# Performance work log

Hardware: AMD Instinct MI355X
Metric: run time of the kernel (lower is better)

The kernel has to match this reference:

```python
import jax, jax.numpy as jnp
import numpy as np

B, S, E, H = 4, 2048, 1024, 16
D = E // H
N_INF = -10000.0


def setup_inputs() -> dict:
    key = jax.random.key(0)
    ks = jax.random.split(key, 12)
    sc = 1.0 / np.sqrt(E)
    inp = {
        "q": jax.random.normal(ks[0], (B, S, E), jnp.float32),
        "k": jax.random.normal(ks[1], (B, S, E), jnp.float32),
        "v": jax.random.normal(ks[2], (B, S, E), jnp.float32),
        "mask": jax.random.randint(ks[3], (1, 1, S, S), 0, 2, jnp.int32),
        "wq": jax.random.normal(ks[4], (E, E), jnp.float32) * sc,
        "bq": jax.random.normal(ks[5], (E,), jnp.float32) * sc,
        "wk": jax.random.normal(ks[6], (E, E), jnp.float32) * sc,
        "bk": jax.random.normal(ks[7], (E,), jnp.float32) * sc,
        "wv": jax.random.normal(ks[8], (E, E), jnp.float32) * sc,
        "bv": jax.random.normal(ks[9], (E,), jnp.float32) * sc,
        "wo": jax.random.normal(ks[10], (E, E), jnp.float32) * sc,
        "bo": jax.random.normal(ks[11], (E,), jnp.float32) * sc,
    }
    return inp


def _split(x):
    # [B,S,E] -> [B,H,S,D]
    return x.reshape(B, S, H, D).transpose(0, 2, 1, 3)


def reference(q, k, v, mask, wq, bq, wk, bk, wv, bv, wo, bo):
    # Linear projections (torch Linear: x @ W^T + b)
    qh = _split(q @ wq.T + bq)
    kh = _split(k @ wk.T + bk)
    vh = _split(v @ wv.T + bv)
    # scaled dot-product attention
    scores = jnp.einsum("bhqd,bhkd->bhqk", qh, kh) / jnp.sqrt(jnp.float32(D))
    scores = jnp.where(mask == 0, jnp.float32(N_INF), scores)
    attn = jax.nn.softmax(scores, axis=-1)
    out = jnp.einsum("bhqk,bhkd->bhqd", attn, vh)
    # concat heads: [B,H,S,D] -> [B,S,E]
    out = out.transpose(0, 2, 1, 3).reshape(B, S, E)
    return out @ wo.T + bo
```

## Files before the change

### kernel.cpp

```cpp
#include <hip/hip_runtime.h>

typedef __attribute__((ext_vector_type(8))) short short8;
typedef __attribute__((ext_vector_type(4))) short s16x4;
typedef __attribute__((ext_vector_type(4))) float f32x4;
typedef __attribute__((ext_vector_type(4))) int int4v;
typedef __attribute__((ext_vector_type(2))) unsigned int uint2v;
typedef __attribute__((ext_vector_type(4))) unsigned int uint4v;

#define MFMA16x16x32(a, b, c) __builtin_amdgcn_mfma_f32_16x16x32_bf16((a), (b), (c), 0, 0, 0)

#define QK_SCALE 0.18033688011112042f

__device__ __forceinline__ unsigned short f2bf(float f) {
  unsigned u = __builtin_bit_cast(unsigned, f);
  u += 0x7fffu + ((u >> 16) & 1u);
  return (unsigned short)(u >> 16);
}

__device__ __forceinline__ unsigned cvt_pk(float lo, float hi) {
  unsigned r;
  asm("v_cvt_pk_bf16_f32 %0, %1, %2" : "=v"(r) : "v"(lo), "v"(hi));
  return r;
}

__device__ __forceinline__ f32x4 mfma16(s16x4 a, s16x4 b, f32x4 c) {
  f32x4 d;
  asm("v_mfma_f32_16x16x16_bf16 %0, %1, %2, %3" : "=v"(d) : "v"(a), "v"(b), "v"(c));
  return d;
}

__global__ __launch_bounds__(256) void prep_bf16(const float* __restrict__ in,
                                                 unsigned short* __restrict__ out) {
  const int i = (blockIdx.x * 256 + threadIdx.x) * 8;
  f32x4 a = *(const f32x4*)(in + i);
  f32x4 b = *(const f32x4*)(in + i + 4);
  uint4v r;
  r[0] = cvt_pk(a[0], a[1]);
  r[1] = cvt_pk(a[2], a[3]);
  r[2] = cvt_pk(b[0], b[1]);
  r[3] = cvt_pk(b[2], b[3]);
  *(uint4v*)(out + i) = r;
}

__global__ __launch_bounds__(256) void prep_biasf(const int* __restrict__ mask,
                                                  float* __restrict__ bias) {
  const int i = (blockIdx.x * 256 + threadIdx.x) * 8;
  int4v m0 = *(const int4v*)(mask + i);
  int4v m1 = *(const int4v*)(mask + i + 4);
  f32x4 o0, o1;
#pragma unroll
  for (int j = 0; j < 4; ++j) o0[j] = (m0[j] == 0) ? -96.0f : 0.0f;
#pragma unroll
  for (int j = 0; j < 4; ++j) o1[j] = (m1[j] == 0) ? -96.0f : 0.0f;
  *(f32x4*)(bias + i) = o0;
  *(f32x4*)(bias + i + 4) = o1;
}

template <int EPI>
__global__ __launch_bounds__(256) void gemm_bt(
    const unsigned short* __restrict__ A, const unsigned short* __restrict__ B,
    const float* __restrict__ bias, void* __restrict__ out,
    int M, int N, int K, float scl) {
  __shared__ unsigned short Asm[128][72];
  __shared__ unsigned short Bsm[128][72];
  const int tid = threadIdx.x;
  const int lane = tid & 63;
  const int wid = tid >> 6;
  const int wr = wid >> 1, wc = wid & 1;
  const int mbase = blockIdx.y * 128, nbase = blockIdx.x * 128;

  f32x4 acc[4][4] = {};

  for (int k0 = 0; k0 < K; k0 += 64) {
#pragma unroll
    for (int r = 0; r < 4; ++r) {
      const int c = tid + 256 * r;
      const int row = c >> 3, col = (c & 7) << 3;
      *(short8*)&Asm[row][col] = *(const short8*)(A + (size_t)(mbase + row) * K + k0 + col);
      *(short8*)&Bsm[row][col] = *(const short8*)(B + (size_t)(nbase + row) * K + k0 + col);
    }
    __syncthreads();
#pragma unroll
    for (int ks = 0; ks < 2; ++ks) {
      const int kk = ks * 32 + (lane >> 4) * 8;
      short8 af[4], bfv[4];
#pragma unroll
      for (int t = 0; t < 4; ++t) {
        af[t] = *(const short8*)&Asm[wr * 64 + t * 16 + (lane & 15)][kk];
        bfv[t] = *(const short8*)&Bsm[wc * 64 + t * 16 + (lane & 15)][kk];
      }
#pragma unroll
      for (int tm = 0; tm < 4; ++tm)
#pragma unroll
        for (int tn = 0; tn < 4; ++tn)
          acc[tm][tn] = MFMA16x16x32(af[tm], bfv[tn], acc[tm][tn]);
    }
    __syncthreads();
  }

  float bn[4];
  if (EPI == 0 || EPI == 2) {
#pragma unroll
    for (int tn = 0; tn < 4; ++tn)
      bn[tn] = bias[nbase + wc * 64 + tn * 16 + (lane & 15)];
  }
  float bm[4][4];
  if (EPI == 1) {
#pragma unroll
    for (int tm = 0; tm < 4; ++tm)
#pragma unroll
      for (int i = 0; i < 4; ++i)
        bm[tm][i] = bias[mbase + wr * 64 + tm * 16 + (lane >> 4) * 4 + i];
  }
#pragma unroll
  for (int tm = 0; tm < 4; ++tm) {
#pragma unroll
    for (int i = 0; i < 4; ++i) {
      const int m = mbase + wr * 64 + tm * 16 + (lane >> 4) * 4 + i;
#pragma unroll
      for (int tn = 0; tn < 4; ++tn) {
        const int n = nbase + wc * 64 + tn * 16 + (lane & 15);
        const float v = (acc[tm][tn][i] + (EPI == 1 ? bm[tm][i] : bn[tn])) * scl;
        if (EPI == 0) {
          const size_t idx =
              (((size_t)(m >> 11) * 16 + (n >> 6)) * 2048 + (m & 2047)) * 64 + (n & 63);
          ((unsigned short*)out)[idx] = f2bf(v);
        } else if (EPI == 1) {
          const size_t idx =
              (((size_t)(n >> 11) * 16 + (m >> 6)) * 64 + (m & 63)) * 2048 + (n & 2047);
          ((unsigned short*)out)[idx] = f2bf(v);
        } else {
          ((float*)out)[(size_t)m * N + n] = v;
        }
      }
    }
  }
}

__global__ __launch_bounds__(256, 4) void attn_fused(
    const unsigned short* __restrict__ Qh, const unsigned short* __restrict__ Kh,
    const unsigned short* __restrict__ VT, const float* __restrict__ Biasf,
    unsigned short* __restrict__ Ob) {
  __shared__ unsigned short Kl[64][72];
  __shared__ unsigned short Vl[64][72];
  const int tid = threadIdx.x, lane = tid & 63, w = tid >> 6;
  const int m = lane & 15, g = lane >> 4;
  const int wg = ((blockIdx.x & 7) << 7) + (blockIdx.x >> 3);
  const int qt = wg & 15, bh = wg >> 4;
  const int q0 = qt << 7;
  const unsigned short* Qb = Qh + (size_t)bh * (2048 * 64);
  const unsigned short* Kb = Kh + (size_t)bh * (2048 * 64);
  const unsigned short* Vb = VT + (size_t)bh * (64 * 2048);

  short8 qf[2][2];
#pragma unroll
  for (int ks = 0; ks < 2; ++ks)
#pragma unroll
    for (int tq = 0; tq < 2; ++tq)
      qf[ks][tq] = *(const short8*)(Qb +
          (size_t)(q0 + w * 32 + tq * 16 + m) * 64 + ks * 32 + g * 8);

  const float* brow[2];
#pragma unroll
  for (int tq = 0; tq < 2; ++tq)
    brow[tq] = Biasf + (size_t)(q0 + w * 32 + tq * 16 + m) * 2048 + g * 4;

  f32x4 acc[2][4] = {};
  float l_run[2] = {0.f, 0.f};

  for (int kt = 0; kt < 32; ++kt) {
    const int kv0 = kt << 6;
    __syncthreads();
#pragma unroll
    for (int r = 0; r < 2; ++r) {
      const int c = tid + 256 * r;
      const int row = c >> 3, col = (c & 7) << 3;
      *(short8*)&Kl[row][col] = *(const short8*)(Kb + (size_t)(kv0 + row) * 64 + col);
      *(short8*)&Vl[row][col] = *(const short8*)(Vb + (size_t)row * 2048 + kv0 + col);
    }
    f32x4 bini[2][4];
#pragma unroll
    for (int tq = 0; tq < 2; ++tq)
#pragma unroll
      for (int tkv = 0; tkv < 4; ++tkv)
        bini[tq][tkv] = *(const f32x4*)(brow[tq] + kv0 + tkv * 16);
    __syncthreads();

    f32x4 st[4][2];
#pragma unroll
    for (int tkv = 0; tkv < 4; ++tkv)
#pragma unroll
      for (int tq = 0; tq < 2; ++tq) st[tkv][tq] = bini[tq][tkv];
    __builtin_amdgcn_s_setprio(1);
#pragma unroll
    for (int ks = 0; ks < 2; ++ks) {
      const int kk = ks * 32 + g * 8;
      short8 kf[4];
#pragma unroll
      for (int t = 0; t < 4; ++t) kf[t] = *(const short8*)&Kl[t * 16 + m][kk];
#pragma unroll
      for (int tkv = 0; tkv < 4; ++tkv)
#pragma unroll
        for (int tq = 0; tq < 2; ++tq)
          st[tkv][tq] = MFMA16x16x32(kf[tkv], qf[ks][tq], st[tkv][tq]);
    }
    __builtin_amdgcn_s_setprio(0);

    uint2v pa[2][4];
#pragma unroll
    for (int tq = 0; tq < 2; ++tq) {
      float rsum = l_run[tq];
#pragma unroll
      for (int tkv = 0; tkv < 4; ++tkv) {
        const float x0 = __builtin_amdgcn_exp2f(st[tkv][tq][0]);
        const float x1 = __builtin_amdgcn_exp2f(st[tkv][tq][1]);
        const float x2 = __builtin_amdgcn_exp2f(st[tkv][tq][2]);
        const float x3 = __builtin_amdgcn_exp2f(st[tkv][tq][3]);
        rsum += (x0 + x1) + (x2 + x3);
        pa[tq][tkv][0] = cvt_pk(x0, x1);
        pa[tq][tkv][1] = cvt_pk(x2, x3);
      }
      l_run[tq] = rsum;
    }

    asm volatile("s_nop 1");
    __builtin_amdgcn_s_setprio(1);
#pragma unroll
    for (int tn = 0; tn < 4; ++tn) {
      s16x4 vf[4];
#pragma unroll
      for (int tkv = 0; tkv < 4; ++tkv)
        vf[tkv] = *(const s16x4*)&Vl[tn * 16 + m][tkv * 16 + g * 4];
#pragma unroll
      for (int tm = 0; tm < 2; ++tm)
#pragma unroll
        for (int tkv = 0; tkv < 4; ++tkv)
          acc[tm][tn] = mfma16(__builtin_bit_cast(s16x4, pa[tm][tkv]), vf[tkv], acc[tm][tn]);
    }
    __builtin_amdgcn_s_setprio(0);
  }

  asm volatile("s_nop 7\ns_nop 7");

#pragma unroll
  for (int tm = 0; tm < 2; ++tm) {
    l_run[tm] += __shfl_xor(l_run[tm], 16);
    l_run[tm] += __shfl_xor(l_run[tm], 32);
  }

  const int b = bh >> 4, h = bh & 15;
#pragma unroll
  for (int tm = 0; tm < 2; ++tm) {
#pragma unroll
    for (int i = 0; i < 4; ++i) {
      const float lv = __shfl(l_run[tm], (g << 2) + i);
      const float rl = 1.0f / lv;
      const int q = q0 + w * 32 + tm * 16 + (g << 2) + i;
      unsigned short* orow = Ob + ((size_t)b * 2048 + q) * 1024 + h * 64;
#pragma unroll
      for (int tn = 0; tn < 4; ++tn)
        orow[tn * 16 + m] = f2bf(acc[tm][tn][i] * rl);
    }
  }
}

extern "C" void kernel_launch(void* const* d_in, const int* in_sizes, int n_in,
                              void* d_out, int out_size, void* d_ws, size_t ws_size,
                              hipStream_t stream) {
  const float* q = (const float*)d_in[0];
  const float* k = (const float*)d_in[1];
  const float* v = (const float*)d_in[2];
  const int* mask = (const int*)d_in[3];
  const float* wq = (const float*)d_in[4];
  const float* bq = (const float*)d_in[5];
  const float* wk = (const float*)d_in[6];
  const float* bk = (const float*)d_in[7];
  const float* wv = (const float*)d_in[8];
  const float* bv = (const float*)d_in[9];
  const float* wo = (const float*)d_in[10];
  const float* bo = (const float*)d_in[11];

  char* ws = (char*)d_ws;
  unsigned short* Qh = (unsigned short*)ws;
  unsigned short* Kh = (unsigned short*)(ws + (16u << 20));
  unsigned short* VT = (unsigned short*)(ws + (32u << 20));
  float* Biasf = (float*)(ws + (48u << 20));
  unsigned short* S = (unsigned short*)(ws + (64u << 20));
  unsigned short* Ob = S;
  unsigned short* wqb = Kh;
  unsigned short* wkb = VT;
  unsigned short* wvb = (unsigned short*)Biasf;
  unsigned short* wob = Qh;

  const dim3 blk(256);
  prep_bf16<<<dim3(4096), blk, 0, stream>>>(q, S);
  prep_bf16<<<dim3(512), blk, 0, stream>>>(wq, wqb);
  gemm_bt<0><<<dim3(8, 64), blk, 0, stream>>>(S, wqb, bq, (void*)Qh, 8192, 1024, 1024, QK_SCALE);
  prep_bf16<<<dim3(4096), blk, 0, stream>>>(k, S);
  prep_bf16<<<dim3(512), blk, 0, stream>>>(wk, wkb);
  gemm_bt<0><<<dim3(8, 64), blk, 0, stream>>>(S, wkb, bk, (void*)Kh, 8192, 1024, 1024, 1.0f);
  prep_bf16<<<dim3(4096), blk, 0, stream>>>(v, S);
  prep_bf16<<<dim3(512), blk, 0, stream>>>(wv, wvb);
  gemm_bt<1><<<dim3(64, 8), blk, 0, stream>>>(wvb, S, bv, (void*)VT, 1024, 8192, 1024, 1.0f);
  prep_biasf<<<dim3(2048), blk, 0, stream>>>(mask, Biasf);
  attn_fused<<<dim3(1024), blk, 0, stream>>>(Qh, Kh, VT, Biasf, Ob);
  prep_bf16<<<dim3(512), blk, 0, stream>>>(wo, wob);
  gemm_bt<2><<<dim3(8, 64), blk, 0, stream>>>(Ob, wob, bo, d_out, 8192, 1024, 1024, 1.0f);
}
```

Before: 301.2 us.

## Prefetch GEMM tiles in registers, double-buffer attention K/V, halve query tile

The GEMM now loads the next K-slice of A and B into registers while the current slice is being multiplied, so global load latency overlaps with MFMA work. The attention kernel double-buffers K/V in shared memory with a register prefetch two tiles ahead, prefetches the next mask-bias tile, and needs one barrier per iteration instead of two. Each attention block now handles 64 query rows instead of 128, with a 2048-block grid. This doubles K/V reloads per head and raises register and LDS use per block, which may lower occupancy.

Result: slower. 309.9 us (+2.9%).

```diff
diff --git a/kernel.cpp b/kernel.cpp
--- a/kernel.cpp
+++ b/kernel.cpp
@@ -68,16 +68,29 @@
   const int wid = tid >> 6;
   const int wr = wid >> 1, wc = wid & 1;
   const int mbase = blockIdx.y * 128, nbase = blockIdx.x * 128;
+  const int srow = tid >> 3, scol = (tid & 7) << 3;
 
   f32x4 acc[4][4] = {};
 
+  short8 areg[4], breg[4];
+#pragma unroll
+  for (int r = 0; r < 4; ++r) {
+    areg[r] = *(const short8*)(A + (size_t)(mbase + srow + 32 * r) * K + scol);
+    breg[r] = *(const short8*)(B + (size_t)(nbase + srow + 32 * r) * K + scol);
+  }
+
   for (int k0 = 0; k0 < K; k0 += 64) {
 #pragma unroll
     for (int r = 0; r < 4; ++r) {
-      const int c = tid + 256 * r;
-      const int row = c >> 3, col = (c & 7) << 3;
-      *(short8*)&Asm[row][col] = *(const short8*)(A + (size_t)(mbase + row) * K + k0 + col);
-      *(short8*)&Bsm[row][col] = *(const short8*)(B + (size_t)(nbase + row) * K + k0 + col);
+      *(short8*)&Asm[srow + 32 * r][scol] = areg[r];
+      *(short8*)&Bsm[srow + 32 * r][scol] = breg[r];
+    }
+    if (k0 + 64 < K) {
+#pragma unroll
+      for (int r = 0; r < 4; ++r) {
+        areg[r] = *(const short8*)(A + (size_t)(mbase + srow + 32 * r) * K + k0 + 64 + scol);
+        breg[r] = *(const short8*)(B + (size_t)(nbase + srow + 32 * r) * K + k0 + 64 + scol);
+      }
     }
     __syncthreads();
 #pragma unroll
@@ -141,87 +154,82 @@
     const unsigned short* __restrict__ Qh, const unsigned short* __restrict__ Kh,
     const unsigned short* __restrict__ VT, const float* __restrict__ Biasf,
     unsigned short* __restrict__ Ob) {
-  __shared__ unsigned short Kl[64][72];
-  __shared__ unsigned short Vl[64][72];
+  __shared__ unsigned short Kl[2][64][72];
+  __shared__ unsigned short Vl[2][64][72];
   const int tid = threadIdx.x, lane = tid & 63, w = tid >> 6;
   const int m = lane & 15, g = lane >> 4;
-  const int wg = ((blockIdx.x & 7) << 7) + (blockIdx.x >> 3);
-  const int qt = wg & 15, bh = wg >> 4;
-  const int q0 = qt << 7;
+  const int wg = ((blockIdx.x & 7) << 8) | (blockIdx.x >> 3);
+  const int qt = wg & 31, bh = wg >> 5;
+  const int q0 = qt << 6;
   const unsigned short* Qb = Qh + (size_t)bh * (2048 * 64);
   const unsigned short* Kb = Kh + (size_t)bh * (2048 * 64);
   const unsigned short* Vb = VT + (size_t)bh * (64 * 2048);
-
-  short8 qf[2][2];
+  const int srow = tid >> 3, scol = (tid & 7) << 3;
+
+  short8 qf[2];
 #pragma unroll
   for (int ks = 0; ks < 2; ++ks)
-#pragma unroll
-    for (int tq = 0; tq < 2; ++tq)
-      qf[ks][tq] = *(const short8*)(Qb +
-          (size_t)(q0 + w * 32 + tq * 16 + m) * 64 + ks * 32 + g * 8);
-
-  const float* brow[2];
-#pragma unroll
-  for (int tq = 0; tq < 2; ++tq)
-    brow[tq] = Biasf + (size_t)(q0 + w * 32 + tq * 16 + m) * 2048 + g * 4;
-
-  f32x4 acc[2][4] = {};
-  float l_run[2] = {0.f, 0.f};
+    qf[ks] = *(const short8*)(Qb + (size_t)(q0 + w * 16 + m) * 64 + ks * 32 + g * 8);
+
+  const float* brow = Biasf + (size_t)(q0 + w * 16 + m) * 2048 + g * 4;
+
+  f32x4 acc[4] = {};
+  float l_run = 0.f;
+
+  short8 kreg[2], vreg[2];
+  kreg[0] = *(const short8*)(Kb + (size_t)srow * 64 + scol);
+  kreg[1] = *(const short8*)(Kb + (size_t)(srow + 32) * 64 + scol);
+  vreg[0] = *(const short8*)(Vb + (size_t)srow * 2048 + scol);
+  vreg[1] = *(const short8*)(Vb + (size_t)(srow + 32) * 2048 + scol);
+  f32x4 bini[4];
+#pragma unroll
+  for (int tkv = 0; tkv < 4; ++tkv) bini[tkv] = *(const f32x4*)(brow + tkv * 16);
+  *(short8*)&Kl[0][srow][scol] = kreg[0];
+  *(short8*)&Kl[0][srow + 32][scol] = kreg[1];
+  *(short8*)&Vl[0][srow][scol] = vreg[0];
+  *(short8*)&Vl[0][srow + 32][scol] = vreg[1];
+  kreg[0] = *(const short8*)(Kb + (size_t)(64 + srow) * 64 + scol);
+  kreg[1] = *(const short8*)(Kb + (size_t)(64 + srow + 32) * 64 + scol);
+  vreg[0] = *(const short8*)(Vb + (size_t)srow * 2048 + 64 + scol);
+  vreg[1] = *(const short8*)(Vb + (size_t)(srow + 32) * 2048 + 64 + scol);
+  __syncthreads();
 
   for (int kt = 0; kt < 32; ++kt) {
-    const int kv0 = kt << 6;
-    __syncthreads();
-#pragma unroll
-    for (int r = 0; r < 2; ++r) {
-      const int c = tid + 256 * r;
-      const int row = c >> 3, col = (c & 7) << 3;
-      *(short8*)&Kl[row][col] = *(const short8*)(Kb + (size_t)(kv0 + row) * 64 + col);
-      *(short8*)&Vl[row][col] = *(const short8*)(Vb + (size_t)row * 2048 + kv0 + col);
-    }
-    f32x4 bini[2][4];
-#pragma unroll
-    for (int tq = 0; tq < 2; ++tq)
+    const int buf = kt & 1;
+    f32x4 st[4];
+#pragma unroll
+    for (int tkv = 0; tkv < 4; ++tkv) st[tkv] = bini[tkv];
+    if (kt < 31) {
 #pragma unroll
       for (int tkv = 0; tkv < 4; ++tkv)
-        bini[tq][tkv] = *(const f32x4*)(brow[tq] + kv0 + tkv * 16);
-    __syncthreads();
-
-    f32x4 st[4][2];
-#pragma unroll
-    for (int tkv = 0; tkv < 4; ++tkv)
-#pragma unroll
-      for (int tq = 0; tq < 2; ++tq) st[tkv][tq] = bini[tq][tkv];
+        bini[tkv] = *(const f32x4*)(brow + (kt + 1) * 64 + tkv * 16);
+    }
     __builtin_amdgcn_s_setprio(1);
 #pragma unroll
     for (int ks = 0; ks < 2; ++ks) {
       const int kk = ks * 32 + g * 8;
       short8 kf[4];
 #pragma unroll
-      for (int t = 0; t < 4; ++t) kf[t] = *(const short8*)&Kl[t * 16 + m][kk];
+      for (int t = 0; t < 4; ++t) kf[t] = *(const short8*)&Kl[buf][t * 16 + m][kk];
 #pragma unroll
       for (int tkv = 0; tkv < 4; ++tkv)
-#pragma unroll
-        for (int tq = 0; tq < 2; ++tq)
-          st[tkv][tq] = MFMA16x16x32(kf[tkv], qf[ks][tq], st[tkv][tq]);
+        st[tkv] = MFMA16x16x32(kf[tkv], qf[ks], st[tkv]);
     }
     __builtin_amdgcn_s_setprio(0);
 
-    uint2v pa[2][4];
-#pragma unroll
-    for (int tq = 0; tq < 2; ++tq) {
-      float rsum = l_run[tq];
-#pragma unroll
-      for (int tkv = 0; tkv < 4; ++tkv) {
-        const float x0 = __builtin_amdgcn_exp2f(st[tkv][tq][0]);
-        const float x1 = __builtin_amdgcn_exp2f(st[tkv][tq][1]);
-        const float x2 = __builtin_amdgcn_exp2f(st[tkv][tq][2]);
-        const float x3 = __builtin_amdgcn_exp2f(st[tkv][tq][3]);
-        rsum += (x0 + x1) + (x2 + x3);
-        pa[tq][tkv][0] = cvt_pk(x0, x1);
-        pa[tq][tkv][1] = cvt_pk(x2, x3);
-      }
-      l_run[tq] = rsum;
-    }
+    uint2v pa[4];
+    float rsum = l_run;
+#pragma unroll
+    for (int tkv = 0; tkv < 4; ++tkv) {
+      const float x0 = __builtin_amdgcn_exp2f(st[tkv][0]);
+      const float x1 = __builtin_amdgcn_exp2f(st[tkv][1]);
+      const float x2 = __builtin_amdgcn_exp2f(st[tkv][2]);
+      const float x3 = __builtin_amdgcn_exp2f(st[tkv][3]);
+      rsum += (x0 + x1) + (x2 + x3);
+      pa[tkv][0] = cvt_pk(x0, x1);
+      pa[tkv][1] = cvt_pk(x2, x3);
+    }
+    l_run = rsum;
 
     asm volatile("s_nop 1");
     __builtin_amdgcn_s_setprio(1);
@@ -230,37 +238,44 @@
       s16x4 vf[4];
 #pragma unroll
       for (int tkv = 0; tkv < 4; ++tkv)
-        vf[tkv] = *(const s16x4*)&Vl[tn * 16 + m][tkv * 16 + g * 4];
-#pragma unroll
-      for (int tm = 0; tm < 2; ++tm)
-#pragma unroll
-        for (int tkv = 0; tkv < 4; ++tkv)
-          acc[tm][tn] = mfma16(__builtin_bit_cast(s16x4, pa[tm][tkv]), vf[tkv], acc[tm][tn]);
+        vf[tkv] = *(const s16x4*)&Vl[buf][tn * 16 + m][tkv * 16 + g * 4];
+#pragma unroll
+      for (int tkv = 0; tkv < 4; ++tkv)
+        acc[tn] = mfma16(__builtin_bit_cast(s16x4, pa[tkv]), vf[tkv], acc[tn]);
     }
     __builtin_amdgcn_s_setprio(0);
+
+    if (kt < 31) {
+      *(short8*)&Kl[buf ^ 1][srow][scol] = kreg[0];
+      *(short8*)&Kl[buf ^ 1][srow + 32][scol] = kreg[1];
+      *(short8*)&Vl[buf ^ 1][srow][scol] = vreg[0];
+      *(short8*)&Vl[buf ^ 1][srow + 32][scol] = vreg[1];
+      if (kt < 30) {
+        const int kv2 = (kt + 2) << 6;
+        kreg[0] = *(const short8*)(Kb + (size_t)(kv2 + srow) * 64 + scol);
+        kreg[1] = *(const short8*)(Kb + (size_t)(kv2 + srow + 32) * 64 + scol);
+        vreg[0] = *(const short8*)(Vb + (size_t)srow * 2048 + kv2 + scol);
+        vreg[1] = *(const short8*)(Vb + (size_t)(srow + 32) * 2048 + kv2 + scol);
+      }
+    }
+    __syncthreads();
   }
 
   asm volatile("s_nop 7\ns_nop 7");
 
-#pragma unroll
-  for (int tm = 0; tm < 2; ++tm) {
-    l_run[tm] += __shfl_xor(l_run[tm], 16);
-    l_run[tm] += __shfl_xor(l_run[tm], 32);
-  }
+  l_run += __shfl_xor(l_run, 16);
+  l_run += __shfl_xor(l_run, 32);
 
   const int b = bh >> 4, h = bh & 15;
 #pragma unroll
-  for (int tm = 0; tm < 2; ++tm) {
-#pragma unroll
-    for (int i = 0; i < 4; ++i) {
-      const float lv = __shfl(l_run[tm], (g << 2) + i);
-      const float rl = 1.0f / lv;
-      const int q = q0 + w * 32 + tm * 16 + (g << 2) + i;
-      unsigned short* orow = Ob + ((size_t)b * 2048 + q) * 1024 + h * 64;
-#pragma unroll
-      for (int tn = 0; tn < 4; ++tn)
-        orow[tn * 16 + m] = f2bf(acc[tm][tn][i] * rl);
-    }
+  for (int i = 0; i < 4; ++i) {
+    const float lv = __shfl(l_run, (g << 2) + i);
+    const float rl = 1.0f / lv;
+    const int q = q0 + w * 16 + (g << 2) + i;
+    unsigned short* orow = Ob + ((size_t)b * 2048 + q) * 1024 + h * 64;
+#pragma unroll
+    for (int tn = 0; tn < 4; ++tn)
+      orow[tn * 16 + m] = f2bf(acc[tn][i] * rl);
   }
 }
 
@@ -303,7 +318,7 @@
   prep_bf16<<<dim3(512), blk, 0, stream>>>(wv, wvb);
   gemm_bt<1><<<dim3(64, 8), blk, 0, stream>>>(wvb, S, bv, (void*)VT, 1024, 8192, 1024, 1.0f);
   prep_biasf<<<dim3(2048), blk, 0, stream>>>(mask, Biasf);
-  attn_fused<<<dim3(1024), blk, 0, stream>>>(Qh, Kh, VT, Biasf, Ob);
+  attn_fused<<<dim3(2048), blk, 0, stream>>>(Qh, Kh, VT, Biasf, Ob);
   prep_bf16<<<dim3(512), blk, 0, stream>>>(wo, wob);
   gemm_bt<2><<<dim3(8, 64), blk, 0, stream>>>(Ob, wob, bo, d_out, 8192, 1024, 1024, 1.0f);
 }
```

## Prefetch GEMM tiles into registers and double-buffer K/V in attention

Applied to the files above, without the earlier changes.

The GEMM kernel now preloads the next K-slice of A and B into registers while the current tile is computed, so global load latency overlaps the MFMA work. The attention kernel double-buffers K/V tiles in LDS with a two-stage register prefetch, which leaves one barrier per iteration instead of two. The mask bias is also added after the QK MFMA rather than used as the accumulator's starting value, so the bias loads no longer have to finish before the MFMAs start. In exchange it uses more registers and doubles attention LDS, which may reduce occupancy under the 4-wave launch bound.

Measured after the change: 445.3 us. 1.48x slower.

```diff
diff --git a/kernel.cpp b/kernel.cpp
--- a/kernel.cpp
+++ b/kernel.cpp
@@ -68,16 +68,29 @@
   const int wid = tid >> 6;
   const int wr = wid >> 1, wc = wid & 1;
   const int mbase = blockIdx.y * 128, nbase = blockIdx.x * 128;
+  const int srow = tid >> 3, scol = (tid & 7) << 3;
 
   f32x4 acc[4][4] = {};
 
+  short8 areg[4], breg[4];
+#pragma unroll
+  for (int r = 0; r < 4; ++r) {
+    areg[r] = *(const short8*)(A + (size_t)(mbase + srow + 32 * r) * K + scol);
+    breg[r] = *(const short8*)(B + (size_t)(nbase + srow + 32 * r) * K + scol);
+  }
+
   for (int k0 = 0; k0 < K; k0 += 64) {
 #pragma unroll
     for (int r = 0; r < 4; ++r) {
-      const int c = tid + 256 * r;
-      const int row = c >> 3, col = (c & 7) << 3;
-      *(short8*)&Asm[row][col] = *(const short8*)(A + (size_t)(mbase + row) * K + k0 + col);
-      *(short8*)&Bsm[row][col] = *(const short8*)(B + (size_t)(nbase + row) * K + k0 + col);
+      *(short8*)&Asm[srow + 32 * r][scol] = areg[r];
+      *(short8*)&Bsm[srow + 32 * r][scol] = breg[r];
+    }
+    if (k0 + 64 < K) {
+#pragma unroll
+      for (int r = 0; r < 4; ++r) {
+        areg[r] = *(const short8*)(A + (size_t)(mbase + srow + 32 * r) * K + k0 + 64 + scol);
+        breg[r] = *(const short8*)(B + (size_t)(nbase + srow + 32 * r) * K + k0 + 64 + scol);
+      }
     }
     __syncthreads();
 #pragma unroll
@@ -141,8 +154,8 @@
     const unsigned short* __restrict__ Qh, const unsigned short* __restrict__ Kh,
     const unsigned short* __restrict__ VT, const float* __restrict__ Biasf,
     unsigned short* __restrict__ Ob) {
-  __shared__ unsigned short Kl[64][72];
-  __shared__ unsigned short Vl[64][72];
+  __shared__ unsigned short Kl[2][64][72];
+  __shared__ unsigned short Vl[2][64][72];
   const int tid = threadIdx.x, lane = tid & 63, w = tid >> 6;
   const int m = lane & 15, g = lane >> 4;
   const int wg = ((blockIdx.x & 7) << 7) + (blockIdx.x >> 3);
@@ -151,6 +164,7 @@
   const unsigned short* Qb = Qh + (size_t)bh * (2048 * 64);
   const unsigned short* Kb = Kh + (size_t)bh * (2048 * 64);
   const unsigned short* Vb = VT + (size_t)bh * (64 * 2048);
+  const int srow = tid >> 3, scol = (tid & 7) << 3;
 
   short8 qf[2][2];
 #pragma unroll
@@ -168,36 +182,40 @@
   f32x4 acc[2][4] = {};
   float l_run[2] = {0.f, 0.f};
 
+  short8 kreg[2], vreg[2];
+  kreg[0] = *(const short8*)(Kb + (size_t)srow * 64 + scol);
+  kreg[1] = *(const short8*)(Kb + (size_t)(srow + 32) * 64 + scol);
+  vreg[0] = *(const short8*)(Vb + (size_t)srow * 2048 + scol);
+  vreg[1] = *(const short8*)(Vb + (size_t)(srow + 32) * 2048 + scol);
+  *(short8*)&Kl[0][srow][scol] = kreg[0];
+  *(short8*)&Kl[0][srow + 32][scol] = kreg[1];
+  *(short8*)&Vl[0][srow][scol] = vreg[0];
+  *(short8*)&Vl[0][srow + 32][scol] = vreg[1];
+  kreg[0] = *(const short8*)(Kb + (size_t)(64 + srow) * 64 + scol);
+  kreg[1] = *(const short8*)(Kb + (size_t)(64 + srow + 32) * 64 + scol);
+  vreg[0] = *(const short8*)(Vb + (size_t)srow * 2048 + 64 + scol);
+  vreg[1] = *(const short8*)(Vb + (size_t)(srow + 32) * 2048 + 64 + scol);
+  __syncthreads();
+
   for (int kt = 0; kt < 32; ++kt) {
+    const int buf = kt & 1;
     const int kv0 = kt << 6;
-    __syncthreads();
-#pragma unroll
-    for (int r = 0; r < 2; ++r) {
-      const int c = tid + 256 * r;
-      const int row = c >> 3, col = (c & 7) << 3;
-      *(short8*)&Kl[row][col] = *(const short8*)(Kb + (size_t)(kv0 + row) * 64 + col);
-      *(short8*)&Vl[row][col] = *(const short8*)(Vb + (size_t)row * 2048 + kv0 + col);
-    }
+
     f32x4 bini[2][4];
 #pragma unroll
     for (int tq = 0; tq < 2; ++tq)
 #pragma unroll
       for (int tkv = 0; tkv < 4; ++tkv)
         bini[tq][tkv] = *(const f32x4*)(brow[tq] + kv0 + tkv * 16);
-    __syncthreads();
-
-    f32x4 st[4][2];
-#pragma unroll
-    for (int tkv = 0; tkv < 4; ++tkv)
-#pragma unroll
-      for (int tq = 0; tq < 2; ++tq) st[tkv][tq] = bini[tq][tkv];
+
+    f32x4 st[4][2] = {};
     __builtin_amdgcn_s_setprio(1);
 #pragma unroll
     for (int ks = 0; ks < 2; ++ks) {
       const int kk = ks * 32 + g * 8;
       short8 kf[4];
 #pragma unroll
-      for (int t = 0; t < 4; ++t) kf[t] = *(const short8*)&Kl[t * 16 + m][kk];
+      for (int t = 0; t < 4; ++t) kf[t] = *(const short8*)&Kl[buf][t * 16 + m][kk];
 #pragma unroll
       for (int tkv = 0; tkv < 4; ++tkv)
 #pragma unroll
@@ -212,10 +230,10 @@
       float rsum = l_run[tq];
 #pragma unroll
       for (int tkv = 0; tkv < 4; ++tkv) {
-        const float x0 = __builtin_amdgcn_exp2f(st[tkv][tq][0]);
-        const float x1 = __builtin_amdgcn_exp2f(st[tkv][tq][1]);
-        const float x2 = __builtin_amdgcn_exp2f(st[tkv][tq][2]);
-        const float x3 = __builtin_amdgcn_exp2f(st[tkv][tq][3]);
+        const float x0 = __builtin_amdgcn_exp2f(st[tkv][tq][0] + bini[tq][tkv][0]);
+        const float x1 = __builtin_amdgcn_exp2f(st[tkv][tq][1] + bini[tq][tkv][1]);
+        const float x2 = __builtin_amdgcn_exp2f(st[tkv][tq][2] + bini[tq][tkv][2]);
+        const float x3 = __builtin_amdgcn_exp2f(st[tkv][tq][3] + bini[tq][tkv][3]);
         rsum += (x0 + x1) + (x2 + x3);
         pa[tq][tkv][0] = cvt_pk(x0, x1);
         pa[tq][tkv][1] = cvt_pk(x2, x3);
@@ -230,7 +248,7 @@
       s16x4 vf[4];
 #pragma unroll
       for (int tkv = 0; tkv < 4; ++tkv)
-        vf[tkv] = *(const s16x4*)&Vl[tn * 16 + m][tkv * 16 + g * 4];
+        vf[tkv] = *(const s16x4*)&Vl[buf][tn * 16 + m][tkv * 16 + g * 4];
 #pragma unroll
       for (int tm = 0; tm < 2; ++tm)
 #pragma unroll
@@ -238,6 +256,21 @@
           acc[tm][tn] = mfma16(__builtin_bit_cast(s16x4, pa[tm][tkv]), vf[tkv], acc[tm][tn]);
     }
     __builtin_amdgcn_s_setprio(0);
+
+    if (kt < 31) {
+      *(short8*)&Kl[buf ^ 1][srow][scol] = kreg[0];
+      *(short8*)&Kl[buf ^ 1][srow + 32][scol] = kreg[1];
+      *(short8*)&Vl[buf ^ 1][srow][scol] = vreg[0];
+      *(short8*)&Vl[buf ^ 1][srow + 32][scol] = vreg[1];
+      if (kt < 30) {
+        const int kv2 = (kt + 2) << 6;
+        kreg[0] = *(const short8*)(Kb + (size_t)(kv2 + srow) * 64 + scol);
+        kreg[1] = *(const short8*)(Kb + (size_t)(kv2 + srow + 32) * 64 + scol);
+        vreg[0] = *(const short8*)(Vb + (size_t)srow * 2048 + kv2 + scol);
+        vreg[1] = *(const short8*)(Vb + (size_t)(srow + 32) * 2048 + kv2 + scol);
+      }
+    }
+    __syncthreads();
   }
 
   asm volatile("s_nop 7\ns_nop 7");
```
